# Optimization experiments

Hardware: AMD Instinct MI355X
Metric: run time of the kernel (lower is better)

Reference implementation:

```python
import jax, jax.numpy as jnp
import numpy as np

N, E, G = 50000, 1600000, 64
IN, HID, OUT = 128, 64, 64
NEG_SLOPE = 0.2


def _p(key, shape):
    return jax.random.normal(key, shape, dtype=jnp.float32) * 0.1


def setup_inputs() -> dict:
    key = jax.random.key(0)
    ks = jax.random.split(key, 24)
    inp = {
        "x": jax.random.normal(ks[0], (N, IN), dtype=jnp.float32),
        "edge_index": jax.random.randint(ks[1], (2, E), 0, N),
        "edge_attr": jax.random.uniform(ks[2], (E, 1), dtype=jnp.float32),
        "batch": jnp.sort(jax.random.randint(ks[3], (N,), 0, G)),
        # GATv2 layer 1 (in=128 -> 64, heads=1)
        "Wl1": _p(ks[4], (IN, HID)), "bl1": _p(ks[5], (HID,)),
        "Wr1": _p(ks[6], (IN, HID)), "br1": _p(ks[7], (HID,)),
        "We1": _p(ks[8], (1, HID)), "att1": _p(ks[9], (HID,)), "bias1": _p(ks[10], (HID,)),
        # GATv2 layer 2 (64 -> 64)
        "Wl2": _p(ks[11], (HID, OUT)), "bl2": _p(ks[12], (OUT,)),
        "Wr2": _p(ks[13], (HID, OUT)), "br2": _p(ks[14], (OUT,)),
        "We2": _p(ks[15], (1, OUT)), "att2": _p(ks[16], (OUT,)), "bias2": _p(ks[17], (OUT,)),
        # MLP head: fc1 (64->32), bn1 (32), fc3 (32->1)
        "W_fc1": _p(ks[18], (OUT, OUT // 2)), "b_fc1": _p(ks[19], (OUT // 2,)),
        "bn_gamma": jnp.ones((OUT // 2,), jnp.float32),
        "bn_beta": jnp.zeros((OUT // 2,), jnp.float32),
        "bn_mean": _p(ks[20], (OUT // 2,)),
        "bn_var": jax.random.uniform(ks[21], (OUT // 2,), jnp.float32, 0.5, 1.5),
        "W_fc3": _p(ks[22], (OUT // 2, 1)), "b_fc3": _p(ks[23], (1,)),
    }
    return inp


def _add_self_loops(src, dst, edge_attr, n):
    # PyG add_self_loops with fill_value='mean': loop attr = mean of incoming edge attrs per node
    s = jax.ops.segment_sum(edge_attr, dst, num_segments=n)  # (N,1)
    c = jax.ops.segment_sum(jnp.ones((edge_attr.shape[0], 1), edge_attr.dtype), dst, num_segments=n)
    loop_attr = s / jnp.maximum(c, 1.0)
    loops = jnp.arange(n)
    return (jnp.concatenate([src, loops]), jnp.concatenate([dst, loops]),
            jnp.concatenate([edge_attr, loop_attr], axis=0))


def _gatv2(h, src, dst, e_attr, Wl, bl, Wr, br, We, att, bias, n):
    xl = h @ Wl + bl                     # (N, C) source transform
    xr = h @ Wr + br                     # (N, C) target transform
    ef = e_attr @ We                     # (E', C)
    s = jax.nn.leaky_relu(xl[src] + xr[dst] + ef, NEG_SLOPE)  # (E', C)
    logits = s @ att                     # (E',)
    m = jax.ops.segment_max(logits, dst, num_segments=n)
    m = jnp.where(jnp.isfinite(m), m, 0.0)
    p = jnp.exp(logits - m[dst])
    denom = jax.ops.segment_sum(p, dst, num_segments=n)
    alpha = p / (denom[dst] + 1e-16)
    out = jax.ops.segment_sum(alpha[:, None] * xl[src], dst, num_segments=n)
    return out + bias


def reference(x, edge_index, edge_attr, batch,
              Wl1, bl1, Wr1, br1, We1, att1, bias1,
              Wl2, bl2, Wr2, br2, We2, att2, bias2,
              W_fc1, b_fc1, bn_gamma, bn_beta, bn_mean, bn_var, W_fc3, b_fc3):
    n = x.shape[0]
    src, dst, ea = _add_self_loops(edge_index[0], edge_index[1], edge_attr, n)
    h = jax.nn.elu(_gatv2(x, src, dst, ea, Wl1, bl1, Wr1, br1, We1, att1, bias1, n))
    h = jax.nn.elu(_gatv2(h, src, dst, ea, Wl2, bl2, Wr2, br2, We2, att2, bias2, n))
    # global_mean_pool
    sums = jax.ops.segment_sum(h, batch, num_segments=G)
    cnts = jax.ops.segment_sum(jnp.ones((n, 1), h.dtype), batch, num_segments=G)
    pooled = sums / jnp.maximum(cnts, 1.0)
    # head: bn1(relu(fc1(.))) with eval-mode BN, dropout off, then fc3
    z = jax.nn.relu(pooled @ W_fc1 + b_fc1)
    z = (z - bn_mean) / jnp.sqrt(bn_var + 1e-5) * bn_gamma + bn_beta
    return z @ W_fc3 + b_fc3
```

## Files before the change

kernel.cpp:

```cpp
#include <hip/hip_runtime.h>
#include <hip/hip_fp16.h>
#include <math.h>

typedef unsigned long long u64;
typedef __attribute__((ext_vector_type(2))) _Float16 half2v;
typedef __attribute__((ext_vector_type(4))) _Float16 half4v;


#define CAP     12032
#define MAXSPAN 12288
#define PEPB    4096

__device__ __forceinline__ void xf_block(
        const float* __restrict__ h, int ld,
        const float* __restrict__ Wl, const float* __restrict__ bl,
        const float* __restrict__ Wr, const float* __restrict__ br,
        __half* __restrict__ xl, __half* __restrict__ xr,
        int N, int node0, _Float16* rows, int t) {
    int in_dim = 1 << ld;
    int q = in_dim >> 2;
    for (int idx = t; idx < 64 * q; idx += 256) {
        int nn = idx >> (ld - 2);
        int kk = (idx & (q - 1)) << 2;
        int node = node0 + nn;
        float4 v = {0.f, 0.f, 0.f, 0.f};
        if (node < N) v = *(const float4*)(h + (((size_t)node) << ld) + kk);
        half4v hv = {(_Float16)v.x, (_Float16)v.y, (_Float16)v.z, (_Float16)v.w};
        *(half4v*)(rows + (nn << ld) + kk) = hv;
    }
    __syncthreads();
    int lane = t & 63, w = t >> 6;
    int nb = w * 16;
    float al[16], ar[16];
    float blv = bl[lane], brv = br[lane];
#pragma unroll
    for (int i = 0; i < 16; ++i) { al[i] = blv; ar[i] = brv; }
    for (int k = 0; k < in_dim; k += 4) {
        float wl0 = Wl[(k + 0) * 64 + lane], wl1 = Wl[(k + 1) * 64 + lane];
        float wl2 = Wl[(k + 2) * 64 + lane], wl3 = Wl[(k + 3) * 64 + lane];
        float wr0 = Wr[(k + 0) * 64 + lane], wr1 = Wr[(k + 1) * 64 + lane];
        float wr2 = Wr[(k + 2) * 64 + lane], wr3 = Wr[(k + 3) * 64 + lane];
#pragma unroll
        for (int i = 0; i < 16; ++i) {
            half4v r = *(const half4v*)(rows + ((nb + i) << ld) + k);
            al[i] = fmaf((float)r.x, wl0, al[i]); al[i] = fmaf((float)r.y, wl1, al[i]);
            al[i] = fmaf((float)r.z, wl2, al[i]); al[i] = fmaf((float)r.w, wl3, al[i]);
            ar[i] = fmaf((float)r.x, wr0, ar[i]); ar[i] = fmaf((float)r.y, wr1, ar[i]);
            ar[i] = fmaf((float)r.z, wr2, ar[i]); ar[i] = fmaf((float)r.w, wr3, ar[i]);
        }
    }
#pragma unroll
    for (int i = 0; i < 16; ++i) {
        int node = node0 + nb + i;
        if (node < N) {
            xl[((size_t)node << 6) + lane] = __float2half(al[i]);
            xr[((size_t)node << 6) + lane] = __float2half(ar[i]);
        }
    }
}

union XfPartSmem {
    _Float16 rows[64 * 128];
    struct { int lh[256]; int lbase[256]; int lcur[256]; } p;
};

__global__ void k_xf1_part(
        const float* __restrict__ h, int ld,
        const float* __restrict__ Wl, const float* __restrict__ bl,
        const float* __restrict__ Wr, const float* __restrict__ br,
        __half* __restrict__ xl, __half* __restrict__ xr, int N, int nbXF,
        const int* __restrict__ ei, const float* __restrict__ ea,
        int* __restrict__ qtail, u64* __restrict__ queue, int E) {
    __shared__ XfPartSmem sm;
    int t = threadIdx.x;
    if (blockIdx.x < nbXF) {
        xf_block(h, ld, Wl, bl, Wr, br, xl, xr, N, blockIdx.x * 64, sm.rows, t);
    } else {
        int pb = blockIdx.x - nbXF;
        sm.p.lh[t] = 0; sm.p.lcur[t] = 0;
        __syncthreads();
        int base = pb * PEPB;
        int end = base + PEPB; if (end > E) end = E;
        for (int e = base + t; e < end; e += 256) {
            int d = ei[E + e];
            atomicAdd(&sm.p.lh[d >> 8], 1);
        }
        __syncthreads();
        if (sm.p.lh[t]) sm.p.lbase[t] = atomicAdd(&qtail[t], sm.p.lh[t]);
        __syncthreads();
        for (int e = base + t; e < end; e += 256) {
            int d = ei[E + e];
            int src = ei[e];
            float a = ea[e];
            int b = d >> 8;
            int idx = atomicAdd(&sm.p.lcur[b], 1);
            unsigned aq = (unsigned)(a * 16777216.0f);
            queue[(size_t)b * CAP + sm.p.lbase[b] + idx] =
                (((u64)aq) << 25) | (((u64)(d & 255)) << 17) | (unsigned)src;
        }
    }
}

__device__ __forceinline__ unsigned attr_q15(float a) {
    unsigned short hb = __builtin_bit_cast(unsigned short, (_Float16)a);
    return (unsigned)(hb >> 1);
}

__global__ void __launch_bounds__(1024)
k_build(const u64* __restrict__ queue, const int* __restrict__ qtail,
        u64* __restrict__ rs2, unsigned* __restrict__ csr, int N) {
    __shared__ u64 stat[256];
    __shared__ int fill[256], sc[256];
    __shared__ unsigned lcsr[MAXSPAN];
    int t = threadIdx.x, b = blockIdx.x;
    if (t < 256) stat[t] = 0;
    __syncthreads();
    int cnt = qtail[b];
    size_t q0 = (size_t)b * CAP;
    for (int i = t; i < cnt; i += 1024) {
        u64 r = queue[q0 + i];
        int dl = (int)((r >> 17) & 255);
        atomicAdd(&stat[dl], (1ULL << 32) | (unsigned)(r >> 25));
    }
    __syncthreads();
    int dg = (b << 8) + t;
    u64 p = (t < 256) ? stat[t] : 0;
    int deg = (int)(p >> 32);
    int v = (t < 256 && dg < N) ? deg + 1 : 0;
    if (t < 256) sc[t] = v;
    __syncthreads();
    for (int off = 1; off < 256; off <<= 1) {
        int a = (t >= off && t < 256) ? sc[t - off] : 0;
        __syncthreads();
        if (t < 256) sc[t] += a;
        __syncthreads();
    }
    int c0 = b * MAXSPAN;
    if (t < 256 && dg < N) {
        int basel = sc[t] - v;
        rs2[dg] = (u64)(unsigned)(c0 + basel) | (((u64)(unsigned)(c0 + basel + deg + 1)) << 32);
        fill[t] = basel;
        float mean = ((float)(unsigned)p * (1.0f / 16777216.0f)) / fmaxf((float)deg, 1.0f);
        if (basel + deg < MAXSPAN) lcsr[basel + deg] = (attr_q15(mean) << 17) | (unsigned)dg;
    }
    __syncthreads();
    for (int i = t; i < cnt; i += 1024) {
        u64 r = queue[q0 + i];
        int dl = (int)((r >> 17) & 255);
        int pos = atomicAdd(&fill[dl], 1);
        float av = (float)(unsigned)(r >> 25) * (1.0f / 16777216.0f);
        if (pos < MAXSPAN) lcsr[pos] = (attr_q15(av) << 17) | (unsigned)(r & 0x1FFFFu);
    }
    __syncthreads();
    int span = sc[255];
    if (span > MAXSPAN) span = MAXSPAN;
    for (int j = t; j < span; j += 1024) csr[c0 + j] = lcsr[j];
}

__global__ void k_node_xf(const float* __restrict__ h, int ld,
                          const float* __restrict__ Wl, const float* __restrict__ bl,
                          const float* __restrict__ Wr, const float* __restrict__ br,
                          __half* __restrict__ xl, __half* __restrict__ xr, int N) {
    __shared__ _Float16 rows[64 * 64];
    xf_block(h, ld, Wl, bl, Wr, br, xl, xr, N, blockIdx.x * 64, rows, threadIdx.x);
}

#define EDGE_GROUP(r, xh, cc)                                                  \
    {                                                                          \
        _Float16 ah = __builtin_bit_cast(_Float16, (unsigned short)((r >> 16) & 0xFFFEu)); \
        half2v aa = {ah, ah};                                                  \
        half2v x01 = {xh.x, xh.y}, x23 = {xh.z, xh.w};                         \
        half2v v01 = aa * We01 + (x01 + xr01);                                 \
        half2v v23 = aa * We23 + (x23 + xr23);                                 \
        half2v s01 = __builtin_elementwise_max(v01, v01 * k02);                \
        half2v s23 = __builtin_elementwise_max(v23, v23 * k02);                \
        cc = __builtin_amdgcn_fdot2(s01, at01, 0.f, false);                    \
        cc = __builtin_amdgcn_fdot2(s23, at23, cc, false);                     \
    }

__global__ void k_attn(const __half* __restrict__ xl, const __half* __restrict__ xr,
                       const unsigned* __restrict__ csr, const u64* __restrict__ rs2,
                       const float* __restrict__ We, const float* __restrict__ att,
                       const float* __restrict__ bias,
                       float* __restrict__ hout, int N) {
    int lane = threadIdx.x & 63;
    int d = (int)(((size_t)blockIdx.x * blockDim.x + threadIdx.x) >> 6);
    if (d >= N) return;
    int eq = lane >> 4;
    int fl = lane & 15;
    float4 Wef  = *(const float4*)(We + fl * 4);
    float4 attf = *(const float4*)(att + fl * 4);
    half2v We01 = {(_Float16)Wef.x, (_Float16)Wef.y};
    half2v We23 = {(_Float16)Wef.z, (_Float16)Wef.w};
    half2v at01 = {(_Float16)attf.x, (_Float16)attf.y};
    half2v at23 = {(_Float16)attf.z, (_Float16)attf.w};
    half4v xrh = *(const half4v*)(xr + ((size_t)d << 6) + fl * 4);
    half2v xr01 = {xrh.x, xrh.y}, xr23 = {xrh.z, xrh.w};
    const half2v k02 = {(_Float16)0.2f, (_Float16)0.2f};
    u64 rr = rs2[d];
    int e0 = __builtin_amdgcn_readfirstlane((int)(unsigned)rr);
    int e1 = __builtin_amdgcn_readfirstlane((int)(unsigned)(rr >> 32));
    float l = 0.f;
    float4 O = {0.f, 0.f, 0.f, 0.f};
    int e = e0;
    for (; e + 16 <= e1; e += 16) {
        unsigned rA = csr[e + eq];
        unsigned rB = csr[e + 4 + eq];
        unsigned rC = csr[e + 8 + eq];
        unsigned rD = csr[e + 12 + eq];
        half4v xA = *(const half4v*)(xl + (((size_t)(rA & 0x1FFFFu)) << 6) + fl * 4);
        half4v xB = *(const half4v*)(xl + (((size_t)(rB & 0x1FFFFu)) << 6) + fl * 4);
        half4v xC = *(const half4v*)(xl + (((size_t)(rC & 0x1FFFFu)) << 6) + fl * 4);
        half4v xD = *(const half4v*)(xl + (((size_t)(rD & 0x1FFFFu)) << 6) + fl * 4);
        float cA, cB, cC, cD;
        EDGE_GROUP(rA, xA, cA);
        EDGE_GROUP(rB, xB, cB);
        EDGE_GROUP(rC, xC, cC);
        EDGE_GROUP(rD, xD, cD);
#pragma unroll
        for (int mm = 1; mm <= 8; mm <<= 1) {
            cA += __shfl_xor(cA, mm, 64);
            cB += __shfl_xor(cB, mm, 64);
            cC += __shfl_xor(cC, mm, 64);
            cD += __shfl_xor(cD, mm, 64);
        }
        float qA = __expf(cA), qB = __expf(cB), qC = __expf(cC), qD = __expf(cD);
        l += (qA + qB) + (qC + qD);
        O.x = fmaf(qA, (float)xA.x, O.x); O.x = fmaf(qB, (float)xB.x, O.x);
        O.x = fmaf(qC, (float)xC.x, O.x); O.x = fmaf(qD, (float)xD.x, O.x);
        O.y = fmaf(qA, (float)xA.y, O.y); O.y = fmaf(qB, (float)xB.y, O.y);
        O.y = fmaf(qC, (float)xC.y, O.y); O.y = fmaf(qD, (float)xD.y, O.y);
        O.z = fmaf(qA, (float)xA.z, O.z); O.z = fmaf(qB, (float)xB.z, O.z);
        O.z = fmaf(qC, (float)xC.z, O.z); O.z = fmaf(qD, (float)xD.z, O.z);
        O.w = fmaf(qA, (float)xA.w, O.w); O.w = fmaf(qB, (float)xB.w, O.w);
        O.w = fmaf(qC, (float)xC.w, O.w); O.w = fmaf(qD, (float)xD.w, O.w);
    }
    for (; e < e1; e += 4) {
        int ee = e + eq;
        bool valid = ee < e1;
        unsigned r = csr[valid ? ee : (e1 - 1)];
        half4v xh = *(const half4v*)(xl + (((size_t)(r & 0x1FFFFu)) << 6) + fl * 4);
        float c;
        EDGE_GROUP(r, xh, c);
#pragma unroll
        for (int mm = 1; mm <= 8; mm <<= 1) c += __shfl_xor(c, mm, 64);
        float q = valid ? __expf(c) : 0.f;
        l += q;
        O.x = fmaf(q, (float)xh.x, O.x);
        O.y = fmaf(q, (float)xh.y, O.y);
        O.z = fmaf(q, (float)xh.z, O.z);
        O.w = fmaf(q, (float)xh.w, O.w);
    }
#pragma unroll
    for (int mm = 16; mm <= 32; mm <<= 1) {
        l   += __shfl_xor(l, mm, 64);
        O.x += __shfl_xor(O.x, mm, 64);
        O.y += __shfl_xor(O.y, mm, 64);
        O.z += __shfl_xor(O.z, mm, 64);
        O.w += __shfl_xor(O.w, mm, 64);
    }
    if (eq == 0) {
        float inv = 1.0f / (l + 1e-16f);
        float4 b4 = *(const float4*)(bias + fl * 4);
        float4 res;
        res.x = fmaf(O.x, inv, b4.x);
        res.y = fmaf(O.y, inv, b4.y);
        res.z = fmaf(O.z, inv, b4.z);
        res.w = fmaf(O.w, inv, b4.w);
        res.x = res.x > 0.f ? res.x : expm1f(res.x);
        res.y = res.y > 0.f ? res.y : expm1f(res.y);
        res.z = res.z > 0.f ? res.z : expm1f(res.z);
        res.w = res.w > 0.f ? res.w : expm1f(res.w);
        *(float4*)(hout + ((size_t)d << 6) + fl * 4) = res;
    }
}

__global__ void k_pool_head(const float* __restrict__ h, const int* __restrict__ batch,
                            float* __restrict__ pooled, float* __restrict__ gcnt,
                            int N, int npw, int* __restrict__ done,
                            const float* __restrict__ W1, const float* __restrict__ b1,
                            const float* __restrict__ gam, const float* __restrict__ bet,
                            const float* __restrict__ mu, const float* __restrict__ var,
                            const float* __restrict__ W3, const float* __restrict__ b3,
                            float* __restrict__ out, int G) {
    int tid = threadIdx.x;
    int lane = tid & 63;
    int wave = (int)(((size_t)blockIdx.x * blockDim.x + tid) >> 6);
    int begin = wave * npw;
    if (begin < N) {
        int end = begin + npw; if (end > N) end = N;
        int g = batch[begin];
        float acc = 0.f, cnt = 0.f;
        for (int n = begin; n < end; ++n) {
            int gn = batch[n];
            if (gn != g) {
                atomicAdd(&pooled[((size_t)g << 6) + lane], acc);
                if (lane == 0) atomicAdd(&gcnt[g], cnt);
                g = gn; acc = 0.f; cnt = 0.f;
            }
            acc += h[((size_t)n << 6) + lane];
            cnt += 1.f;
        }
        atomicAdd(&pooled[((size_t)g << 6) + lane], acc);
        if (lane == 0) atomicAdd(&gcnt[g], cnt);
    }
    __threadfence();
    __syncthreads();
    __shared__ int lastFlag;
    if (tid == 0) lastFlag = (atomicAdd(done, 1) == (int)gridDim.x - 1);
    __syncthreads();
    if (lastFlag && tid < G) {
        __threadfence();
        int g = tid;
        float inv = 1.0f / fmaxf(gcnt[g], 1.0f);
        float pr[64];
        for (int k = 0; k < 64; ++k) pr[k] = pooled[((size_t)g << 6) + k] * inv;
        float o = b3[0];
        for (int j = 0; j < 32; ++j) {
            float z = b1[j];
            for (int k = 0; k < 64; ++k) z += pr[k] * W1[k * 32 + j];
            z = fmaxf(z, 0.f);
            z = (z - mu[j]) / sqrtf(var[j] + 1e-5f) * gam[j] + bet[j];
            o += z * W3[j];
        }
        out[g] = o;
    }
}

extern "C" void kernel_launch(void* const* d_in, const int* in_sizes, int n_in,
                              void* d_out, int out_size, void* d_ws, size_t ws_size,
                              hipStream_t stream) {
    const float* x    = (const float*)d_in[0];
    const int*   ei   = (const int*)d_in[1];
    const float* ea   = (const float*)d_in[2];
    const int*   batch= (const int*)d_in[3];
    const float* Wl1  = (const float*)d_in[4];
    const float* bl1  = (const float*)d_in[5];
    const float* Wr1  = (const float*)d_in[6];
    const float* br1  = (const float*)d_in[7];
    const float* We1  = (const float*)d_in[8];
    const float* att1 = (const float*)d_in[9];
    const float* bi1  = (const float*)d_in[10];
    const float* Wl2  = (const float*)d_in[11];
    const float* bl2  = (const float*)d_in[12];
    const float* Wr2  = (const float*)d_in[13];
    const float* br2  = (const float*)d_in[14];
    const float* We2  = (const float*)d_in[15];
    const float* att2 = (const float*)d_in[16];
    const float* bi2  = (const float*)d_in[17];
    const float* Wf1  = (const float*)d_in[18];
    const float* bf1  = (const float*)d_in[19];
    const float* gam  = (const float*)d_in[20];
    const float* bet  = (const float*)d_in[21];
    const float* mu   = (const float*)d_in[22];
    const float* var  = (const float*)d_in[23];
    const float* Wf3  = (const float*)d_in[24];
    const float* bf3  = (const float*)d_in[25];

    const int N    = in_sizes[3];
    const int E    = in_sizes[2];
    const int INd  = in_sizes[0] / N;
    const int ld1  = (INd == 128) ? 7 : 6;
    const int G    = out_size;
    const int NB   = (N + 255) / 256;

    char* w = (char*)d_ws;
    auto carve = [&](size_t bytes) { char* p = w; w += (bytes + 255) & ~(size_t)255; return p; };
    __half*   xl       = (__half*)  carve((size_t)N * 64 * 2);
    __half*   xr       = (__half*)  carve((size_t)N * 64 * 2);
    float*    hbuf     = (float*)   carve((size_t)N * 64 * 4);
    unsigned* csr      = (unsigned*)carve((size_t)NB * MAXSPAN * 4);
    u64*      queue    = (u64*)     carve((size_t)NB * CAP * 8);
    u64*      rs2      = (u64*)     carve((size_t)N * 8);
    int*      qtail    = (int*)     carve((size_t)(NB + 1) * 4);
    float*    pooled   = (float*)   carve((size_t)G * 64 * 4);
    float*    gcnt     = (float*)   carve((size_t)G * 4);
    int*      done     = (int*)     carve(256);

    const int TB = 256;
    const int nbXF = (N + 63) / 64;
    const int attnBlocks = (N + 3) / 4;
    const int nbPart = (E + PEPB - 1) / PEPB;

    hipMemsetAsync(qtail, 0, (size_t)(NB + 1) * 4, stream);
    size_t poolRegion = (((size_t)G * 64 * 4 + 255) & ~(size_t)255)
                      + (((size_t)G * 4 + 255) & ~(size_t)255) + 256;
    hipMemsetAsync(pooled, 0, poolRegion, stream);

    k_xf1_part<<<nbXF + nbPart, TB, 0, stream>>>(x, ld1, Wl1, bl1, Wr1, br1, xl, xr, N, nbXF,
                                                 ei, ea, qtail, queue, E);
    k_build<<<NB, 1024, 0, stream>>>(queue, qtail, rs2, csr, N);

    k_attn<<<attnBlocks, TB, 0, stream>>>(xl, xr, csr, rs2, We1, att1, bi1, hbuf, N);

    k_node_xf<<<nbXF, TB, 0, stream>>>(hbuf, 6, Wl2, bl2, Wr2, br2, xl, xr, N);
    k_attn<<<attnBlocks, TB, 0, stream>>>(xl, xr, csr, rs2, We2, att2, bi2, hbuf, N);

    const int npw = 64;
    const int poolWaves = (N + npw - 1) / npw;
    k_pool_head<<<(poolWaves * 64 + TB - 1) / TB, TB, 0, stream>>>(
        hbuf, batch, pooled, gcnt, N, npw, done,
        Wf1, bf1, gam, bet, mu, var, Wf3, bf3, (float*)d_out, G);
}
```

Before: 354.1 us.

## Use MFMA f16 matrix cores for node feature transforms with pre-transposed weights

Replaces the scalar FMA dense transform (xl/xr projections) with MFMA 16x16x32 f16 instructions. A new prep kernel transposes and converts Wl/Wr into a concatenated fp16 [128 x IN] matrix and a merged bias vector, and the row staging buffer is padded to reduce LDS bank conflicts. This targets the compute cost of the two node transform stages, at the cost of an extra small kernel launch and fp16 weights instead of fp32.

Result: faster. 320.7 us (-9.4%).

```diff
diff --git a/kernel.cpp b/kernel.cpp
--- a/kernel.cpp
+++ b/kernel.cpp
@@ -5,76 +5,121 @@
 typedef unsigned long long u64;
 typedef __attribute__((ext_vector_type(2))) _Float16 half2v;
 typedef __attribute__((ext_vector_type(4))) _Float16 half4v;
+typedef __attribute__((ext_vector_type(8))) _Float16 half8;
+typedef __attribute__((ext_vector_type(4))) float f32x4;
 
 
 #define CAP     12032
 #define MAXSPAN 12288
 #define PEPB    4096
 
-__device__ __forceinline__ void xf_block(
-        const float* __restrict__ h, int ld,
-        const float* __restrict__ Wl, const float* __restrict__ bl,
-        const float* __restrict__ Wr, const float* __restrict__ br,
+__global__ void k_prep_w(const float* __restrict__ Wl1, const float* __restrict__ bl1,
+                         const float* __restrict__ Wr1, const float* __restrict__ br1,
+                         const float* __restrict__ Wl2, const float* __restrict__ bl2,
+                         const float* __restrict__ Wr2, const float* __restrict__ br2,
+                         _Float16* __restrict__ Wt1, float* __restrict__ bv1,
+                         _Float16* __restrict__ Wt2, float* __restrict__ bv2, int ld1) {
+    int t = blockIdx.x * blockDim.x + threadIdx.x;
+    int stride = gridDim.x * blockDim.x;
+    int IN1 = 1 << ld1;
+    for (int i = t; i < 128 * IN1; i += stride) {
+        int n = i >> ld1, k = i & (IN1 - 1);
+        float v = (n < 64) ? Wl1[k * 64 + n] : Wr1[k * 64 + (n - 64)];
+        Wt1[n * IN1 + k] = (_Float16)v;
+    }
+    for (int i = t; i < 128 * 64; i += stride) {
+        int n = i >> 6, k = i & 63;
+        float v = (n < 64) ? Wl2[k * 64 + n] : Wr2[k * 64 + (n - 64)];
+        Wt2[n * 64 + k] = (_Float16)v;
+    }
+    if (t < 128) {
+        bv1[t] = (t < 64) ? bl1[t] : br1[t - 64];
+        bv2[t] = (t < 64) ? bl2[t] : br2[t - 64];
+    }
+}
+
+template<int IN>
+__device__ __forceinline__ void xf_block_mfma(
+        const float* __restrict__ h,
+        const _Float16* __restrict__ Wt,
+        const float* __restrict__ bv,
         __half* __restrict__ xl, __half* __restrict__ xr,
         int N, int node0, _Float16* rows, int t) {
-    int in_dim = 1 << ld;
-    int q = in_dim >> 2;
-    for (int idx = t; idx < 64 * q; idx += 256) {
-        int nn = idx >> (ld - 2);
-        int kk = (idx & (q - 1)) << 2;
+    constexpr int LDK = IN + 8;
+    constexpr int Q = IN / 4;
+    for (int idx = t; idx < 64 * Q; idx += 256) {
+        int nn = idx / Q;
+        int kk = (idx % Q) * 4;
         int node = node0 + nn;
         float4 v = {0.f, 0.f, 0.f, 0.f};
-        if (node < N) v = *(const float4*)(h + (((size_t)node) << ld) + kk);
+        if (node < N) v = *(const float4*)(h + (size_t)node * IN + kk);
         half4v hv = {(_Float16)v.x, (_Float16)v.y, (_Float16)v.z, (_Float16)v.w};
-        *(half4v*)(rows + (nn << ld) + kk) = hv;
+        *(half4v*)(rows + nn * LDK + kk) = hv;
     }
     __syncthreads();
     int lane = t & 63, w = t >> 6;
-    int nb = w * 16;
-    float al[16], ar[16];
-    float blv = bl[lane], brv = br[lane];
-#pragma unroll
-    for (int i = 0; i < 16; ++i) { al[i] = blv; ar[i] = brv; }
-    for (int k = 0; k < in_dim; k += 4) {
-        float wl0 = Wl[(k + 0) * 64 + lane], wl1 = Wl[(k + 1) * 64 + lane];
-        float wl2 = Wl[(k + 2) * 64 + lane], wl3 = Wl[(k + 3) * 64 + lane];
-        float wr0 = Wr[(k + 0) * 64 + lane], wr1 = Wr[(k + 1) * 64 + lane];
-        float wr2 = Wr[(k + 2) * 64 + lane], wr3 = Wr[(k + 3) * 64 + lane];
-#pragma unroll
-        for (int i = 0; i < 16; ++i) {
-            half4v r = *(const half4v*)(rows + ((nb + i) << ld) + k);
-            al[i] = fmaf((float)r.x, wl0, al[i]); al[i] = fmaf((float)r.y, wl1, al[i]);
-            al[i] = fmaf((float)r.z, wl2, al[i]); al[i] = fmaf((float)r.w, wl3, al[i]);
-            ar[i] = fmaf((float)r.x, wr0, ar[i]); ar[i] = fmaf((float)r.y, wr1, ar[i]);
-            ar[i] = fmaf((float)r.z, wr2, ar[i]); ar[i] = fmaf((float)r.w, wr3, ar[i]);
-        }
-    }
-#pragma unroll
-    for (int i = 0; i < 16; ++i) {
-        int node = node0 + nb + i;
-        if (node < N) {
-            xl[((size_t)node << 6) + lane] = __float2half(al[i]);
-            xr[((size_t)node << 6) + lane] = __float2half(ar[i]);
+    int n0w = w * 32;
+    int lr = lane & 15, lq = lane >> 4;
+    f32x4 acc[4][2];
+#pragma unroll
+    for (int i = 0; i < 4; ++i)
+#pragma unroll
+        for (int j = 0; j < 2; ++j) acc[i][j] = {0.f, 0.f, 0.f, 0.f};
+    const _Float16* arow = rows + lr * LDK + lq * 8;
+    const _Float16* brow = Wt + (size_t)(n0w + lr) * IN + lq * 8;
+#pragma unroll
+    for (int k0 = 0; k0 < IN; k0 += 32) {
+        half8 a0 = *(const half8*)(arow + k0);
+        half8 a1 = *(const half8*)(arow + 16 * LDK + k0);
+        half8 a2 = *(const half8*)(arow + 32 * LDK + k0);
+        half8 a3 = *(const half8*)(arow + 48 * LDK + k0);
+        half8 b0 = *(const half8*)(brow + k0);
+        half8 b1 = *(const half8*)(brow + 16 * IN + k0);
+        acc[0][0] = __builtin_amdgcn_mfma_f32_16x16x32_f16(a0, b0, acc[0][0], 0, 0, 0);
+        acc[1][0] = __builtin_amdgcn_mfma_f32_16x16x32_f16(a1, b0, acc[1][0], 0, 0, 0);
+        acc[2][0] = __builtin_amdgcn_mfma_f32_16x16x32_f16(a2, b0, acc[2][0], 0, 0, 0);
+        acc[3][0] = __builtin_amdgcn_mfma_f32_16x16x32_f16(a3, b0, acc[3][0], 0, 0, 0);
+        acc[0][1] = __builtin_amdgcn_mfma_f32_16x16x32_f16(a0, b1, acc[0][1], 0, 0, 0);
+        acc[1][1] = __builtin_amdgcn_mfma_f32_16x16x32_f16(a1, b1, acc[1][1], 0, 0, 0);
+        acc[2][1] = __builtin_amdgcn_mfma_f32_16x16x32_f16(a2, b1, acc[2][1], 0, 0, 0);
+        acc[3][1] = __builtin_amdgcn_mfma_f32_16x16x32_f16(a3, b1, acc[3][1], 0, 0, 0);
+    }
+    float bia0 = bv[n0w + lr];
+    float bia1 = bv[n0w + 16 + lr];
+#pragma unroll
+    for (int ni = 0; ni < 2; ++ni) {
+        int dim = n0w + ni * 16 + lr;
+        __half* dst = (dim < 64) ? xl : xr;
+        int dd = dim & 63;
+        float bb = ni ? bia1 : bia0;
+#pragma unroll
+        for (int mi = 0; mi < 4; ++mi) {
+#pragma unroll
+            for (int r = 0; r < 4; ++r) {
+                int node = node0 + mi * 16 + lq * 4 + r;
+                if (node < N)
+                    dst[((size_t)node << 6) + dd] = __float2half(acc[mi][ni][r] + bb);
+            }
         }
     }
 }
 
 union XfPartSmem {
-    _Float16 rows[64 * 128];
+    _Float16 rows[64 * 136];
     struct { int lh[256]; int lbase[256]; int lcur[256]; } p;
 };
 
+template<int IN>
 __global__ void k_xf1_part(
-        const float* __restrict__ h, int ld,
-        const float* __restrict__ Wl, const float* __restrict__ bl,
-        const float* __restrict__ Wr, const float* __restrict__ br,
+        const float* __restrict__ h,
+        const _Float16* __restrict__ Wt, const float* __restrict__ bv,
         __half* __restrict__ xl, __half* __restrict__ xr, int N, int nbXF,
         const int* __restrict__ ei, const float* __restrict__ ea,
         int* __restrict__ qtail, u64* __restrict__ queue, int E) {
     __shared__ XfPartSmem sm;
     int t = threadIdx.x;
     if (blockIdx.x < nbXF) {
-        xf_block(h, ld, Wl, bl, Wr, br, xl, xr, N, blockIdx.x * 64, sm.rows, t);
+        xf_block_mfma<IN>(h, Wt, bv, xl, xr, N, blockIdx.x * 64, sm.rows, t);
     } else {
         int pb = blockIdx.x - nbXF;
         sm.p.lh[t] = 0; sm.p.lcur[t] = 0;
@@ -157,12 +202,11 @@
     for (int j = t; j < span; j += 1024) csr[c0 + j] = lcsr[j];
 }
 
-__global__ void k_node_xf(const float* __restrict__ h, int ld,
-                          const float* __restrict__ Wl, const float* __restrict__ bl,
-                          const float* __restrict__ Wr, const float* __restrict__ br,
+__global__ void k_node_xf(const float* __restrict__ h,
+                          const _Float16* __restrict__ Wt, const float* __restrict__ bv,
                           __half* __restrict__ xl, __half* __restrict__ xr, int N) {
-    __shared__ _Float16 rows[64 * 64];
-    xf_block(h, ld, Wl, bl, Wr, br, xl, xr, N, blockIdx.x * 64, rows, threadIdx.x);
+    __shared__ _Float16 rows[64 * 72];
+    xf_block_mfma<64>(h, Wt, bv, xl, xr, N, blockIdx.x * 64, rows, threadIdx.x);
 }
 
 #define EDGE_GROUP(r, xh, cc)                                                  \
@@ -376,6 +420,10 @@
     float*    pooled   = (float*)   carve((size_t)G * 64 * 4);
     float*    gcnt     = (float*)   carve((size_t)G * 4);
     int*      done     = (int*)     carve(256);
+    _Float16* Wt1      = (_Float16*)carve((size_t)128 * 128 * 2);
+    float*    bv1      = (float*)   carve(128 * 4);
+    _Float16* Wt2      = (_Float16*)carve((size_t)128 * 64 * 2);
+    float*    bv2      = (float*)   carve(128 * 4);
 
     const int TB = 256;
     const int nbXF = (N + 63) / 64;
@@ -387,13 +435,20 @@
                       + (((size_t)G * 4 + 255) & ~(size_t)255) + 256;
     hipMemsetAsync(pooled, 0, poolRegion, stream);
 
-    k_xf1_part<<<nbXF + nbPart, TB, 0, stream>>>(x, ld1, Wl1, bl1, Wr1, br1, xl, xr, N, nbXF,
-                                                 ei, ea, qtail, queue, E);
+    k_prep_w<<<32, TB, 0, stream>>>(Wl1, bl1, Wr1, br1, Wl2, bl2, Wr2, br2,
+                                    Wt1, bv1, Wt2, bv2, ld1);
+
+    if (INd == 128)
+        k_xf1_part<128><<<nbXF + nbPart, TB, 0, stream>>>(x, Wt1, bv1, xl, xr, N, nbXF,
+                                                          ei, ea, qtail, queue, E);
+    else
+        k_xf1_part<64><<<nbXF + nbPart, TB, 0, stream>>>(x, Wt1, bv1, xl, xr, N, nbXF,
+                                                         ei, ea, qtail, queue, E);
     k_build<<<NB, 1024, 0, stream>>>(queue, qtail, rs2, csr, N);
 
     k_attn<<<attnBlocks, TB, 0, stream>>>(xl, xr, csr, rs2, We1, att1, bi1, hbuf, N);
 
-    k_node_xf<<<nbXF, TB, 0, stream>>>(hbuf, 6, Wl2, bl2, Wr2, br2, xl, xr, N);
+    k_node_xf<<<nbXF, TB, 0, stream>>>(hbuf, Wt2, bv2, xl, xr, N);
     k_attn<<<attnBlocks, TB, 0, stream>>>(xl, xr, csr, rs2, We2, att2, bi2, hbuf, N);
 
     const int npw = 64;
```
